# Performance work log

Hardware: AMD Instinct MI355X
Metric: run time of the kernel (lower is better)

The kernel has to match this reference:

```python
import jax, jax.numpy as jnp
import numpy as np

B, H, V, L, M, D, C = 64, 512, 50000, 400, 128, 64, 64
HC = 2 * D + M + 4  # controller LSTM hidden size (one head)
EPS = 1e-8


def _lstm_step(x, h, c, Wih, Whh, bih, bhh):
    g = x @ Wih.T + bih + h @ Whh.T + bhh
    i, f, gg, o = jnp.split(g, 4, axis=-1)
    c2 = jax.nn.sigmoid(f) * c + jax.nn.sigmoid(i) * jnp.tanh(gg)
    return jax.nn.sigmoid(o) * jnp.tanh(c2), c2


def _head_params(hc):
    # slices exactly as in LSTMMemoryController (k=0, single head)
    keys = hc[:, :M]                               # [B, M]
    kstr = jnp.exp(hc[:, D:D + 1])                 # [B, 1]
    gate = jax.nn.sigmoid(hc[:, D + 1:D + 2])      # [B, 1]
    erase = jax.nn.sigmoid(hc[:, D + 4:M + D + 4]) # [B, M]
    add = jax.nn.sigmoid(hc[:, 2 * D + 4:M + 2 * D + 4])  # [B, M]
    return keys, kstr, gate, erase, add


def _addressing(keys, kstr, gate, heads, memory):
    # torch cosine_similarity(keys.unsqueeze(2), memory, dim=2):
    # keys [B,M] broadcast along memory_dim D
    num = keys * memory.sum(-1)                                   # [B, M]
    nk = jnp.maximum(jnp.abs(keys) * jnp.sqrt(jnp.float32(D)), EPS)
    nm = jnp.maximum(jnp.linalg.norm(memory, axis=-1), EPS)
    cos = num / (nk * nm)
    content = jax.nn.softmax(kstr * cos, axis=1)                  # [B, M]
    # faithful to original: heads[k] indexes axis 0 (k=0) -> shape [1, M]
    gated = gate * content + (1.0 - gate) * heads[0]
    return gated[:, None, :]                                      # [B, 1, M]


def reference(input_ids, h0, c0, encoder_outputs, word_occurrence_indicator,
              coverage, memory, read_heads, write_heads,
              read_h, read_c, write_h, write_c,
              emb, attn_W, attn_b, cov_W, state_W, comb_W, comb_b,
              rpre_W, rpre_b, wpre_W, wpre_b,
              r_Wih, r_Whh, r_bih, r_bhh,
              w_Wih, w_Whh, w_bih, w_bhh,
              l_Wih, l_Whh, l_bih, l_bhh,
              out_W, out_b):
    embedded = emb[input_ids]                                     # [B, H]
    ia = jnp.concatenate([embedded, h0], 1) @ attn_W.T + attn_b  # [B, L]
    tc = (coverage + ia) @ cov_W.T
    ts = c0 @ state_W.T
    aw = jax.nn.softmax(tc + ia + ts, axis=1)                     # [B, L]
    attn_applied = jnp.einsum('bl,blh->bh', aw, encoder_outputs)  # [B, H]
    out0 = jnp.concatenate([embedded, attn_applied], 1) @ comb_W.T + comb_b  # [B, H]

    hm = jnp.concatenate([h0, memory.reshape(-1, M * D)], 1)
    rh, rc = _lstm_step(hm @ rpre_W.T + rpre_b, read_h, read_c, r_Wih, r_Whh, r_bih, r_bhh)
    wh, wc = _lstm_step(hm @ wpre_W.T + wpre_b, write_h, write_c, w_Wih, w_Whh, w_bih, w_bhh)
    rk, rks, rg, _, _ = _head_params(rh)
    wk, wks, wg, we, wa = _head_params(wh)
    rw = _addressing(rk, rks, rg, read_heads, memory)             # [B, 1, M]
    ww = _addressing(wk, wks, wg, write_heads, memory)            # [B, 1, M]

    read_in = jnp.einsum('bkm,bmd->bkd', rw, memory).reshape(-1, D)
    h1, c1 = _lstm_step(jnp.concatenate([out0, read_in], 1), h0, c0,
                        l_Wih, l_Whh, l_bih, l_bhh)
    # residual (h1 + out0) is computed in the original but unused by its output path

    w0 = ww[:, 0, :, None]                                        # [B, M, 1]
    new_memory = memory * (1.0 - w0 * we[:, :, None]) + w0 * wa[:, :, None]
    new_coverage = coverage + ia

    log_probs = jax.nn.log_softmax(c1[:, None, :] @ out_W.T + out_b, axis=-1)  # [B, 1, V]
    return log_probs, h1, c1, new_memory, new_coverage


def setup_inputs() -> dict:
    key = jax.random.key(0)
    ks = iter(jax.random.split(key, 48))

    def rn(shape, fan_in):
        return jax.random.normal(next(ks), shape, jnp.float32) / np.sqrt(fan_in)

    inp = {
        'input_ids': jax.random.randint(next(ks), (B,), 0, V),
        'h0': jax.random.normal(next(ks), (B, H), jnp.float32),
        'c0': jax.random.normal(next(ks), (B, H), jnp.float32),
        'encoder_outputs': jax.random.normal(next(ks), (B, L, H), jnp.float32),
        'word_occurrence_indicator': jnp.zeros((B, L), jnp.float32),
        'coverage': jnp.zeros((B, L), jnp.float32),
        'memory': jax.random.normal(next(ks), (B, M, D), jnp.float32),
        'read_heads': jnp.zeros((B, 1, M), jnp.float32),
        'write_heads': jnp.zeros((B, 1, M), jnp.float32),
        'read_h': jnp.zeros((B, HC), jnp.float32),
        'read_c': jnp.zeros((B, HC), jnp.float32),
        'write_h': jnp.zeros((B, HC), jnp.float32),
        'write_c': jnp.zeros((B, HC), jnp.float32),
        'emb': rn((V, H), H),
        'attn_W': rn((L, 2 * H), 2 * H), 'attn_b': jnp.zeros((L,), jnp.float32),
        'cov_W': rn((L, L), L),
        'state_W': rn((L, H), H),
        'comb_W': rn((H, 2 * H), 2 * H), 'comb_b': jnp.zeros((H,), jnp.float32),
        'rpre_W': rn((C, M * D + H), M * D + H), 'rpre_b': jnp.zeros((C,), jnp.float32),
        'wpre_W': rn((C, M * D + H), M * D + H), 'wpre_b': jnp.zeros((C,), jnp.float32),
        'r_Wih': rn((4 * HC, C), C), 'r_Whh': rn((4 * HC, HC), HC),
        'r_bih': jnp.zeros((4 * HC,), jnp.float32), 'r_bhh': jnp.zeros((4 * HC,), jnp.float32),
        'w_Wih': rn((4 * HC, C), C), 'w_Whh': rn((4 * HC, HC), HC),
        'w_bih': jnp.zeros((4 * HC,), jnp.float32), 'w_bhh': jnp.zeros((4 * HC,), jnp.float32),
        'l_Wih': rn((4 * H, H + D), H + D), 'l_Whh': rn((4 * H, H), H),
        'l_bih': jnp.zeros((4 * H,), jnp.float32), 'l_bhh': jnp.zeros((4 * H,), jnp.float32),
        'out_W': rn((V, H), H), 'out_b': jnp.zeros((V,), jnp.float32),
    }
    return inp
```

## Files before the change

kernel.cpp:

```cpp
#include <hip/hip_runtime.h>
#include <math.h>

#define BB 64
#define HH 512
#define VV 50000
#define LL 400
#define MM 128
#define DD 64
#define HC 260
#define EPSF 1e-8f

typedef __attribute__((ext_vector_type(8))) short bf16x8;
typedef __attribute__((ext_vector_type(4))) float f32x4;

__device__ __forceinline__ float sigmoidf(float x){ return 1.0f/(1.0f+expf(-x)); }
__device__ __forceinline__ unsigned short bf16_rne(float f){
  unsigned u = __float_as_uint(f);
  return (unsigned short)((u + 0x7fffu + ((u >> 16) & 1u)) >> 16);
}
__device__ __forceinline__ float wave_max(float v){
  #pragma unroll
  for(int o=32;o;o>>=1) v = fmaxf(v, __shfl_xor(v,o));
  return v;
}
__device__ __forceinline__ float wave_sum(float v){
  #pragma unroll
  for(int o=32;o;o>>=1) v += __shfl_xor(v,o);
  return v;
}

__global__ void k_embed(const int* __restrict__ ids, const float* __restrict__ emb,
                        const float* __restrict__ h0, float* __restrict__ xcat1,
                        float* __restrict__ xcat2){
  int idx = blockIdx.x*256 + threadIdx.x;
  if (idx >= BB*HH) return;
  int b = idx >> 9, h = idx & 511;
  float e = emb[(long)ids[b]*HH + h];
  xcat1[b*1024 + h] = e;
  xcat2[b*1024 + h] = e;
  xcat1[b*1024 + 512 + h] = h0[idx];
}

template<int NB, int FUSE>
__global__ __launch_bounds__(256) void k_gemv(const float* __restrict__ A,
                                              const float* __restrict__ A2,
                                              const float* __restrict__ W,
                                              const float* __restrict__ b1,
                                              float* __restrict__ C,
                                              int K, int N, int ldc){
  int b = blockIdx.y;
  int wid = threadIdx.x >> 6, lane = threadIdx.x & 63;
  int n = blockIdx.x*4 + wid;
  if (n >= N) return;
  const float4* A4  = (const float4*)(A + (long)b*K);
  const float4* A24 = (const float4*)(A2 + (long)b*K);
  const float4* W4  = (const float4*)(W + (long)n*K);
  int K4 = K >> 2;
  float acc = 0.f;
  for (int k = lane; k < K4; k += 64){
    float4 a = A4[k];
    if (FUSE){ float4 a2 = A24[k]; a.x+=a2.x; a.y+=a2.y; a.z+=a2.z; a.w+=a2.w; }
    float4 w = W4[k];
    acc += a.x*w.x + a.y*w.y + a.z*w.z + a.w*w.w;
  }
  acc = wave_sum(acc);
  if (lane == 0){
    if (NB) acc += b1[n];
    C[(long)b*ldc + n] = acc;
  }
}

__global__ void k_cov(const float* __restrict__ cov, const float* __restrict__ ia,
                      float* __restrict__ out){
  int idx = blockIdx.x*256 + threadIdx.x;
  if (idx >= BB*LL) return;
  out[idx] = cov[idx] + ia[idx];
}

__global__ __launch_bounds__(256) void k_softmax_aw(const float* __restrict__ ia,
                                                    const float* __restrict__ ts,
                                                    const float* __restrict__ tc,
                                                    float* __restrict__ aw){
  int b = blockIdx.x, t = threadIdx.x;
  int i0 = t, i1 = t + 256;
  float x0 = ia[b*LL+i0] + ts[b*LL+i0] + tc[b*LL+i0];
  float x1 = (i1 < LL) ? (ia[b*LL+i1] + ts[b*LL+i1] + tc[b*LL+i1]) : -INFINITY;
  __shared__ float sm[4], ss[4];
  float m = wave_max(fmaxf(x0, x1));
  if ((t & 63) == 0) sm[t>>6] = m;
  __syncthreads();
  m = fmaxf(fmaxf(sm[0], sm[1]), fmaxf(sm[2], sm[3]));
  float e0 = expf(x0 - m);
  float e1 = (i1 < LL) ? expf(x1 - m) : 0.0f;
  float s = wave_sum(e0 + e1);
  if ((t & 63) == 0) ss[t>>6] = s;
  __syncthreads();
  float tot = ss[0] + ss[1] + ss[2] + ss[3];
  float inv = 1.0f / tot;
  aw[b*LL + i0] = e0 * inv;
  if (i1 < LL) aw[b*LL + i1] = e1 * inv;
}

__global__ __launch_bounds__(256) void k_attn_part(const float* __restrict__ aw,
                                                   const float* __restrict__ enc,
                                                   float* __restrict__ part){
  int b = blockIdx.x, lc = blockIdx.y, t = threadIdx.x;
  const float* awb = aw + b*LL + lc*25;
  const float* eb  = enc + ((long)b*LL + lc*25)*HH;
  float a0 = 0.f, a1 = 0.f;
  for (int l = 0; l < 25; l++){
    float a = awb[l];
    a0 += a * eb[(long)l*HH + t];
    a1 += a * eb[(long)l*HH + t + 256];
  }
  part[((b*16 + lc) << 9) + t]       = a0;
  part[((b*16 + lc) << 9) + t + 256] = a1;
}

__global__ void k_attn_reduce(const float* __restrict__ part, float* __restrict__ xcat2){
  int idx = blockIdx.x*256 + threadIdx.x;
  if (idx >= BB*HH) return;
  int b = idx >> 9, h = idx & 511;
  float s = 0.f;
  #pragma unroll
  for (int lc = 0; lc < 16; lc++) s += part[((b*16 + lc) << 9) + h];
  xcat2[b*1024 + 512 + h] = s;
}

__global__ __launch_bounds__(256) void k_pre_gemv(const float* __restrict__ h0,
                                                  const float* __restrict__ mem,
                                                  const float* __restrict__ rW,
                                                  const float* __restrict__ wW,
                                                  float* __restrict__ part){
  int wid = threadIdx.x >> 6, lane = threadIdx.x & 63;
  int n = blockIdx.x*4 + wid;
  int b = blockIdx.y;
  int z = blockIdx.z;
  int which = z >> 3, chunk = z & 7;
  const float* W = which ? wW : rW;
  const float4* W4 = (const float4*)(W + (long)n*8704 + chunk*1088);
  const float4* H4 = (const float4*)(h0 + (long)b*HH);
  const float4* M4 = (const float4*)(mem + (long)b*8192 + (chunk*1088 - 512));
  float acc = 0.f;
  #pragma unroll
  for (int i = 0; i < 5; i++){
    int k4 = lane + i*64;
    if (k4 < 272){
      int kg4 = chunk*272 + k4;
      float4 a = (kg4 < 128) ? H4[kg4] : M4[k4];
      float4 w = W4[k4];
      acc += a.x*w.x + a.y*w.y + a.z*w.z + a.w*w.w;
    }
  }
  acc = wave_sum(acc);
  if (lane == 0) part[z*4096 + b*64 + n] = acc;
}

__global__ void k_pre_reduce(const float* __restrict__ part, const float* __restrict__ rb,
                             const float* __restrict__ wb, float* __restrict__ pre_r,
                             float* __restrict__ pre_w){
  int idx = blockIdx.x*256 + threadIdx.x;
  if (idx >= 8192) return;
  int which = idx >> 12;
  int r = idx & 4095;
  float s = 0.f;
  #pragma unroll
  for (int c = 0; c < 8; c++) s += part[((which<<3)+c)*4096 + r];
  int n = r & 63;
  s += which ? wb[n] : rb[n];
  (which ? pre_w : pre_r)[r] = s;
}

__global__ __launch_bounds__(256) void k_gates_rw(const float* __restrict__ pre_r,
    const float* __restrict__ pre_w, const float* __restrict__ read_h,
    const float* __restrict__ write_h,
    const float* __restrict__ rWih, const float* __restrict__ rWhh,
    const float* __restrict__ rbih, const float* __restrict__ rbhh,
    const float* __restrict__ wWih, const float* __restrict__ wWhh,
    const float* __restrict__ wbih, const float* __restrict__ wbhh,
    float* __restrict__ g_r, float* __restrict__ g_w){
  int which = blockIdx.z;
  int b = blockIdx.y;
  int wid = threadIdx.x >> 6, lane = threadIdx.x & 63;
  int n = blockIdx.x*4 + wid;
  const float* pre = which ? pre_w : pre_r;
  const float* hh  = which ? write_h : read_h;
  const float* Wih = which ? wWih : rWih;
  const float* Whh = which ? wWhh : rWhh;
  float acc = pre[b*64 + lane] * Wih[n*64 + lane];
  const float* hb = hh + b*HC;
  const float* wr = Whh + (long)n*HC;
  #pragma unroll
  for (int i = 0; i < 5; i++){
    int k = lane + i*64;
    if (k < HC) acc += hb[k]*wr[k];
  }
  acc = wave_sum(acc);
  if (lane == 0){
    acc += (which ? wbih : rbih)[n] + (which ? wbhh : rbhh)[n];
    (which ? g_w : g_r)[(long)b*4*HC + n] = acc;
  }
}

__global__ void k_lstm_rw(const float* __restrict__ g_r, const float* __restrict__ g_w,
                          const float* __restrict__ read_c, const float* __restrict__ write_c,
                          float* __restrict__ rh, float* __restrict__ wh){
  int idx = blockIdx.x*256 + threadIdx.x;
  if (idx >= 2*BB*HC) return;
  int which = idx >= BB*HC;
  int r = which ? idx - BB*HC : idx;
  int b = r / HC, j = r - b*HC;
  const float* g = (which ? g_w : g_r) + (long)b*4*HC;
  float c2 = sigmoidf(g[HC + j]) * (which ? write_c : read_c)[r]
           + sigmoidf(g[j]) * tanhf(g[2*HC + j]);
  (which ? wh : rh)[r] = sigmoidf(g[3*HC + j]) * tanhf(c2);
}

__global__ __launch_bounds__(128) void k_address(const float* __restrict__ rh,
                                                 const float* __restrict__ whv,
                                                 const float* __restrict__ rheads,
                                                 const float* __restrict__ wheads,
                                                 const float* __restrict__ mem,
                                                 float* __restrict__ rwout,
                                                 float* __restrict__ wwout){
  int which = blockIdx.y;
  int b = blockIdx.x, m = threadIdx.x;
  const float* hc = which ? whv : rh;
  const float* heads0 = which ? wheads : rheads;
  float* wout = which ? wwout : rwout;
  const float* mr = mem + ((long)b*MM + m)*DD;
  float s = 0.f, q = 0.f;
  #pragma unroll 8
  for (int d = 0; d < DD; d++){ float v = mr[d]; s += v; q += v*v; }
  float key  = hc[b*HC + m];
  float kstr = expf(hc[b*HC + 64]);
  float gate = sigmoidf(hc[b*HC + 65]);
  float nk = fmaxf(fabsf(key)*8.0f, EPSF);
  float nm = fmaxf(sqrtf(q), EPSF);
  float z  = kstr * (key*s) / (nk*nm);
  __shared__ float sm[2], ss[2];
  float mx = wave_max(z);
  if ((m & 63) == 0) sm[m>>6] = mx;
  __syncthreads();
  mx = fmaxf(sm[0], sm[1]);
  float e = expf(z - mx);
  float w = wave_sum(e);
  if ((m & 63) == 0) ss[m>>6] = w;
  __syncthreads();
  float content = e / (ss[0] + ss[1]);
  wout[b*MM + m] = gate*content + (1.0f - gate)*heads0[m];
}

__global__ void k_readin(const float* __restrict__ rw, const float* __restrict__ mem,
                         float* __restrict__ xcat3){
  int b = blockIdx.x, d = threadIdx.x;
  float s = 0.f;
  for (int m = 0; m < MM; m++) s += rw[b*MM + m] * mem[((long)b*MM + m)*DD + d];
  xcat3[b*576 + 512 + d] = s;
}

__global__ void k_newmem(const float* __restrict__ mem, const float* __restrict__ ww,
                         const float* __restrict__ wh, float* __restrict__ out){
  int idx = blockIdx.x*256 + threadIdx.x;
  if (idx >= BB*MM*DD) return;
  int b = idx >> 13;
  int m = (idx & 8191) >> 6;
  float w0 = ww[b*MM + m];
  float we = sigmoidf(wh[b*HC + 68 + m]);
  float wa = sigmoidf(wh[b*HC + 132 + m]);
  out[idx] = mem[idx]*(1.0f - w0*we) + w0*wa;
}

__global__ __launch_bounds__(256) void k_lstm_main(const float* __restrict__ xcat3,
                                                   const float* __restrict__ h0,
                                                   const float* __restrict__ lWih,
                                                   const float* __restrict__ lWhh,
                                                   const float* __restrict__ bih,
                                                   const float* __restrict__ bhh,
                                                   const float* __restrict__ c0,
                                                   float* __restrict__ h1,
                                                   float* __restrict__ c1,
                                                   unsigned short* __restrict__ c1b){
  int wid = threadIdx.x >> 6, lane = threadIdx.x & 63;
  int j = blockIdx.x*4 + wid;
  int b = blockIdx.y;
  const float4* A1 = (const float4*)(xcat3 + (long)b*576);
  const float4* A2 = (const float4*)(h0 + (long)b*HH);
  float gv[4];
  #pragma unroll
  for (int g = 0; g < 4; g++){
    int n = g*HH + j;
    const float4* W1 = (const float4*)(lWih + (long)n*576);
    const float4* W2 = (const float4*)(lWhh + (long)n*HH);
    float s = 0.f;
    #pragma unroll
    for (int i = 0; i < 3; i++){
      int k = lane + i*64;
      if (k < 144){ float4 a = A1[k], w = W1[k]; s += a.x*w.x + a.y*w.y + a.z*w.z + a.w*w.w; }
    }
    #pragma unroll
    for (int i = 0; i < 2; i++){
      int k = lane + i*64;
      float4 a = A2[k], w = W2[k]; s += a.x*w.x + a.y*w.y + a.z*w.z + a.w*w.w;
    }
    gv[g] = wave_sum(s);
  }
  if (lane == 0){
    #pragma unroll
    for (int g = 0; g < 4; g++){ int n = g*HH + j; gv[g] += bih[n] + bhh[n]; }
    float c2 = sigmoidf(gv[1])*c0[b*HH + j] + sigmoidf(gv[0])*tanhf(gv[2]);
    h1[b*HH + j] = sigmoidf(gv[3])*tanhf(c2);
    c1[b*HH + j] = c2;
    c1b[b*HH + j] = bf16_rne(c2);
  }
}

__global__ __launch_bounds__(256) void k_logits_mfma(const unsigned short* __restrict__ Ab,
                                                     const float* __restrict__ W,
                                                     const float* __restrict__ bias,
                                                     float* __restrict__ C){
  int wid = threadIdx.x >> 6, lane = threadIdx.x & 63;
  int strip = blockIdx.x*4 + wid;
  if (strip >= 3125) return;
  int nl = lane & 15;
  int q  = lane >> 4;
  int n  = strip*16 + nl;
  const float* wrow = W + (long)n*HH + q*8;
  const unsigned short* a0p = Ab + (0*16 + nl)*HH + q*8;
  const unsigned short* a1p = Ab + (1*16 + nl)*HH + q*8;
  const unsigned short* a2p = Ab + (2*16 + nl)*HH + q*8;
  const unsigned short* a3p = Ab + (3*16 + nl)*HH + q*8;
  f32x4 acc0 = {0.f,0.f,0.f,0.f}, acc1 = acc0, acc2 = acc0, acc3 = acc0;
  #pragma unroll 4
  for (int ks = 0; ks < 16; ks++){
    const float4* wp = (const float4*)(wrow + ks*32);
    float4 w0 = wp[0];
    float4 w1 = wp[1];
    bf16x8 bf;
    bf[0] = (short)bf16_rne(w0.x); bf[1] = (short)bf16_rne(w0.y);
    bf[2] = (short)bf16_rne(w0.z); bf[3] = (short)bf16_rne(w0.w);
    bf[4] = (short)bf16_rne(w1.x); bf[5] = (short)bf16_rne(w1.y);
    bf[6] = (short)bf16_rne(w1.z); bf[7] = (short)bf16_rne(w1.w);
    bf16x8 a0 = *(const bf16x8*)(a0p + ks*32);
    bf16x8 a1 = *(const bf16x8*)(a1p + ks*32);
    bf16x8 a2 = *(const bf16x8*)(a2p + ks*32);
    bf16x8 a3 = *(const bf16x8*)(a3p + ks*32);
    acc0 = __builtin_amdgcn_mfma_f32_16x16x32_bf16(a0, bf, acc0, 0, 0, 0);
    acc1 = __builtin_amdgcn_mfma_f32_16x16x32_bf16(a1, bf, acc1, 0, 0, 0);
    acc2 = __builtin_amdgcn_mfma_f32_16x16x32_bf16(a2, bf, acc2, 0, 0, 0);
    acc3 = __builtin_amdgcn_mfma_f32_16x16x32_bf16(a3, bf, acc3, 0, 0, 0);
  }
  float bv = bias[n];
  #pragma unroll
  for (int r = 0; r < 4; r++){
    int m = q*4 + r;
    C[(long)(m     )*VV + n] = acc0[r] + bv;
    C[(long)(m + 16)*VV + n] = acc1[r] + bv;
    C[(long)(m + 32)*VV + n] = acc2[r] + bv;
    C[(long)(m + 48)*VV + n] = acc3[r] + bv;
  }
}

__global__ __launch_bounds__(256) void k_ls1(const float* __restrict__ lp,
                                             float* __restrict__ pm, float* __restrict__ ps){
  int b = blockIdx.y, c = blockIdx.x, t = threadIdx.x;
  const float* row = lp + (long)b*VV + c*2000;
  float mx = -INFINITY;
  for (int i = t; i < 2000; i += 256) mx = fmaxf(mx, row[i]);
  __shared__ float sm[4], ss[4];
  mx = wave_max(mx);
  if ((t & 63) == 0) sm[t>>6] = mx;
  __syncthreads();
  mx = fmaxf(fmaxf(sm[0], sm[1]), fmaxf(sm[2], sm[3]));
  float s = 0.f;
  for (int i = t; i < 2000; i += 256) s += expf(row[i] - mx);
  s = wave_sum(s);
  if ((t & 63) == 0) ss[t>>6] = s;
  __syncthreads();
  if (t == 0){ pm[b*25 + c] = mx; ps[b*25 + c] = ss[0]+ss[1]+ss[2]+ss[3]; }
}

__global__ void k_ls2(const float* __restrict__ pm, const float* __restrict__ ps,
                      float* __restrict__ lse){
  int b = threadIdx.x;
  float m = -INFINITY;
  for (int c = 0; c < 25; c++) m = fmaxf(m, pm[b*25 + c]);
  float s = 0.f;
  for (int c = 0; c < 25; c++) s += ps[b*25 + c]*expf(pm[b*25 + c] - m);
  lse[b] = m + logf(s);
}

__global__ void k_ls3(float* __restrict__ lp, const float* __restrict__ lse){
  int idx = blockIdx.x*256 + threadIdx.x;
  if (idx >= BB*VV) return;
  int b = idx / VV;
  lp[idx] -= lse[b];
}

extern "C" void kernel_launch(void* const* d_in, const int* in_sizes, int n_in,
                              void* d_out, int out_size, void* d_ws, size_t ws_size,
                              hipStream_t stream) {
  const int*   ids     = (const int*)  d_in[0];
  const float* h0      = (const float*)d_in[1];
  const float* c0      = (const float*)d_in[2];
  const float* enc     = (const float*)d_in[3];
  const float* cov     = (const float*)d_in[5];
  const float* mem     = (const float*)d_in[6];
  const float* rheads  = (const float*)d_in[7];
  const float* wheads  = (const float*)d_in[8];
  const float* read_h  = (const float*)d_in[9];
  const float* read_c  = (const float*)d_in[10];
  const float* write_h = (const float*)d_in[11];
  const float* write_c = (const float*)d_in[12];
  const float* emb     = (const float*)d_in[13];
  const float* attn_W  = (const float*)d_in[14];
  const float* attn_b  = (const float*)d_in[15];
  const float* cov_W   = (const float*)d_in[16];
  const float* state_W = (const float*)d_in[17];
  const float* comb_W  = (const float*)d_in[18];
  const float* comb_b  = (const float*)d_in[19];
  const float* rpre_W  = (const float*)d_in[20];
  const float* rpre_b  = (const float*)d_in[21];
  const float* wpre_W  = (const float*)d_in[22];
  const float* wpre_b  = (const float*)d_in[23];
  const float* r_Wih   = (const float*)d_in[24];
  const float* r_Whh   = (const float*)d_in[25];
  const float* r_bih   = (const float*)d_in[26];
  const float* r_bhh   = (const float*)d_in[27];
  const float* w_Wih   = (const float*)d_in[28];
  const float* w_Whh   = (const float*)d_in[29];
  const float* w_bih   = (const float*)d_in[30];
  const float* w_bhh   = (const float*)d_in[31];
  const float* l_Wih   = (const float*)d_in[32];
  const float* l_Whh   = (const float*)d_in[33];
  const float* l_bih   = (const float*)d_in[34];
  const float* l_bhh   = (const float*)d_in[35];
  const float* out_W   = (const float*)d_in[36];
  const float* out_b   = (const float*)d_in[37];

  float* out  = (float*)d_out;
  float* lp   = out;
  float* h1   = out + 3200000;
  float* c1   = h1 + 32768;
  float* nmem = c1 + 32768;
  float* ncov = nmem + 524288;

  float* w = (float*)d_ws;
  float* xcat1 = w;
  float* xcat2 = xcat1 + 65536;
  float* xcat3 = xcat2 + 65536;
  float* ia    = xcat3 + 36864;
  float* ts    = ia + 25600;
  float* tc    = ts + 25600;
  float* aw    = tc + 25600;
  float* U     = aw + 25600;
  float* pre_r = U + 557056;
  float* pre_w = pre_r + 4096;
  float* g_r   = pre_w + 4096;
  float* g_w   = g_r + 66560;
  float* rh    = g_w + 66560;
  float* wh    = rh + 16640;
  float* rw    = wh + 16640;
  float* wwgt  = rw + 8192;
  float* pm    = wwgt + 8192;
  float* ps    = pm + 1600;
  float* lse   = ps + 1600;
  unsigned short* c1b = (unsigned short*)(lse + 64);

  k_embed<<<128, 256, 0, stream>>>(ids, emb, h0, xcat1, xcat2);
  k_gemv<1,0><<<dim3(100,64), 256, 0, stream>>>(xcat1, xcat1, attn_W, attn_b, ia, 1024, LL, LL);
  k_gemv<0,0><<<dim3(100,64), 256, 0, stream>>>(c0, c0, state_W, nullptr, ts, HH, LL, LL);
  k_cov<<<100, 256, 0, stream>>>(cov, ia, ncov);
  k_gemv<0,1><<<dim3(100,64), 256, 0, stream>>>(cov, ia, cov_W, nullptr, tc, LL, LL, LL);
  k_softmax_aw<<<64, 256, 0, stream>>>(ia, ts, tc, aw);
  k_attn_part<<<dim3(64,16), 256, 0, stream>>>(aw, enc, U);
  k_attn_reduce<<<128, 256, 0, stream>>>(U, xcat2);
  k_gemv<1,0><<<dim3(128,64), 256, 0, stream>>>(xcat2, xcat2, comb_W, comb_b, xcat3, 1024, HH, 576);

  k_pre_gemv<<<dim3(16,64,16), 256, 0, stream>>>(h0, mem, rpre_W, wpre_W, U);
  k_pre_reduce<<<32, 256, 0, stream>>>(U, rpre_b, wpre_b, pre_r, pre_w);

  k_gates_rw<<<dim3(260,64,2), 256, 0, stream>>>(pre_r, pre_w, read_h, write_h,
      r_Wih, r_Whh, r_bih, r_bhh, w_Wih, w_Whh, w_bih, w_bhh, g_r, g_w);
  k_lstm_rw<<<130, 256, 0, stream>>>(g_r, g_w, read_c, write_c, rh, wh);

  k_address<<<dim3(64,2), 128, 0, stream>>>(rh, wh, rheads, wheads, mem, rw, wwgt);
  k_readin<<<64, 64, 0, stream>>>(rw, mem, xcat3);
  k_newmem<<<2048, 256, 0, stream>>>(mem, wwgt, wh, nmem);

  k_lstm_main<<<dim3(128,64), 256, 0, stream>>>(xcat3, h0, l_Wih, l_Whh, l_bih, l_bhh,
                                                c0, h1, c1, c1b);

  k_logits_mfma<<<782, 256, 0, stream>>>(c1b, out_W, out_b, lp);
  k_ls1<<<dim3(25,64), 256, 0, stream>>>(lp, pm, ps);
  k_ls2<<<1, 64, 0, stream>>>(pm, ps, lse);
  k_ls3<<<12500, 256, 0, stream>>>(lp, lse);
}
```

Before: 503.7 us.

## Fuse small kernels, batch gate GEMV, and software-pipeline logits MFMA loads

Folds the coverage update into the attention softmax, merges addressing with the read-in and memory-update kernels, and merges the two-stage log-sum-exp finish into the final subtract kernel, which cuts four launches. The gate GEMV now reuses register-held weights across 8 batch rows per block. The logits MFMA loop prefetches weights and activations two steps ahead with a 3-slot register ring. The trade-offs are more register pressure in the logits kernel and the read-in and memory-update work running on only 128 blocks.

```diff
diff --git a/kernel.cpp b/kernel.cpp
--- a/kernel.cpp
+++ b/kernel.cpp
@@ -70,21 +70,20 @@
   }
 }
 
-__global__ void k_cov(const float* __restrict__ cov, const float* __restrict__ ia,
-                      float* __restrict__ out){
-  int idx = blockIdx.x*256 + threadIdx.x;
-  if (idx >= BB*LL) return;
-  out[idx] = cov[idx] + ia[idx];
-}
-
 __global__ __launch_bounds__(256) void k_softmax_aw(const float* __restrict__ ia,
                                                     const float* __restrict__ ts,
                                                     const float* __restrict__ tc,
-                                                    float* __restrict__ aw){
+                                                    const float* __restrict__ cov,
+                                                    float* __restrict__ aw,
+                                                    float* __restrict__ ncov){
   int b = blockIdx.x, t = threadIdx.x;
   int i0 = t, i1 = t + 256;
-  float x0 = ia[b*LL+i0] + ts[b*LL+i0] + tc[b*LL+i0];
-  float x1 = (i1 < LL) ? (ia[b*LL+i1] + ts[b*LL+i1] + tc[b*LL+i1]) : -INFINITY;
+  float ia0 = ia[b*LL+i0];
+  float x0 = ia0 + ts[b*LL+i0] + tc[b*LL+i0];
+  float ia1 = (i1 < LL) ? ia[b*LL+i1] : 0.f;
+  float x1 = (i1 < LL) ? (ia1 + ts[b*LL+i1] + tc[b*LL+i1]) : -INFINITY;
+  ncov[b*LL + i0] = cov[b*LL + i0] + ia0;
+  if (i1 < LL) ncov[b*LL + i1] = cov[b*LL + i1] + ia1;
   __shared__ float sm[4], ss[4];
   float m = wave_max(fmaxf(x0, x1));
   if ((t & 63) == 0) sm[t>>6] = m;
@@ -180,25 +179,35 @@
     const float* __restrict__ wbih, const float* __restrict__ wbhh,
     float* __restrict__ g_r, float* __restrict__ g_w){
   int which = blockIdx.z;
-  int b = blockIdx.y;
+  int bo = blockIdx.y;
   int wid = threadIdx.x >> 6, lane = threadIdx.x & 63;
   int n = blockIdx.x*4 + wid;
   const float* pre = which ? pre_w : pre_r;
   const float* hh  = which ? write_h : read_h;
   const float* Wih = which ? wWih : rWih;
   const float* Whh = which ? wWhh : rWhh;
-  float acc = pre[b*64 + lane] * Wih[n*64 + lane];
-  const float* hb = hh + b*HC;
+  float* gout = which ? g_w : g_r;
+  float wih_l = Wih[(long)n*64 + lane];
   const float* wr = Whh + (long)n*HC;
+  float whh_l[5];
   #pragma unroll
   for (int i = 0; i < 5; i++){
     int k = lane + i*64;
-    if (k < HC) acc += hb[k]*wr[k];
-  }
-  acc = wave_sum(acc);
-  if (lane == 0){
-    acc += (which ? wbih : rbih)[n] + (which ? wbhh : rbhh)[n];
-    (which ? g_w : g_r)[(long)b*4*HC + n] = acc;
+    whh_l[i] = (k < HC) ? wr[k] : 0.f;
+  }
+  float bsum = (which ? wbih : rbih)[n] + (which ? wbhh : rbhh)[n];
+  #pragma unroll
+  for (int i = 0; i < 8; i++){
+    int b = bo*8 + i;
+    float acc = pre[b*64 + lane] * wih_l;
+    const float* hb = hh + (long)b*HC;
+    #pragma unroll
+    for (int j = 0; j < 5; j++){
+      int k = lane + j*64;
+      if (k < HC) acc += whh_l[j]*hb[k];
+    }
+    acc = wave_sum(acc);
+    if (lane == 0) gout[(long)b*4*HC + n] = acc + bsum;
   }
 }
 
@@ -221,13 +230,12 @@
                                                  const float* __restrict__ rheads,
                                                  const float* __restrict__ wheads,
                                                  const float* __restrict__ mem,
-                                                 float* __restrict__ rwout,
-                                                 float* __restrict__ wwout){
+                                                 float* __restrict__ xcat3,
+                                                 float* __restrict__ nmem){
   int which = blockIdx.y;
   int b = blockIdx.x, m = threadIdx.x;
   const float* hc = which ? whv : rh;
   const float* heads0 = which ? wheads : rheads;
-  float* wout = which ? wwout : rwout;
   const float* mr = mem + ((long)b*MM + m)*DD;
   float s = 0.f, q = 0.f;
   #pragma unroll 8
@@ -239,36 +247,42 @@
   float nm = fmaxf(sqrtf(q), EPSF);
   float z  = kstr * (key*s) / (nk*nm);
   __shared__ float sm[2], ss[2];
+  __shared__ float sw[128];
   float mx = wave_max(z);
   if ((m & 63) == 0) sm[m>>6] = mx;
   __syncthreads();
   mx = fmaxf(sm[0], sm[1]);
   float e = expf(z - mx);
-  float w = wave_sum(e);
-  if ((m & 63) == 0) ss[m>>6] = w;
+  float wsum = wave_sum(e);
+  if ((m & 63) == 0) ss[m>>6] = wsum;
   __syncthreads();
   float content = e / (ss[0] + ss[1]);
-  wout[b*MM + m] = gate*content + (1.0f - gate)*heads0[m];
-}
-
-__global__ void k_readin(const float* __restrict__ rw, const float* __restrict__ mem,
-                         float* __restrict__ xcat3){
-  int b = blockIdx.x, d = threadIdx.x;
-  float s = 0.f;
-  for (int m = 0; m < MM; m++) s += rw[b*MM + m] * mem[((long)b*MM + m)*DD + d];
-  xcat3[b*576 + 512 + d] = s;
-}
-
-__global__ void k_newmem(const float* __restrict__ mem, const float* __restrict__ ww,
-                         const float* __restrict__ wh, float* __restrict__ out){
-  int idx = blockIdx.x*256 + threadIdx.x;
-  if (idx >= BB*MM*DD) return;
-  int b = idx >> 13;
-  int m = (idx & 8191) >> 6;
-  float w0 = ww[b*MM + m];
-  float we = sigmoidf(wh[b*HC + 68 + m]);
-  float wa = sigmoidf(wh[b*HC + 132 + m]);
-  out[idx] = mem[idx]*(1.0f - w0*we) + w0*wa;
+  float w = gate*content + (1.0f - gate)*heads0[m];
+  if (which == 0){
+    sw[m] = w;
+    __syncthreads();
+    if (m < 64){
+      float acc = 0.f;
+      const float* mb = mem + (long)b*MM*DD + m;
+      #pragma unroll 8
+      for (int mm = 0; mm < MM; mm++) acc += sw[mm]*mb[(long)mm*DD];
+      xcat3[b*576 + 512 + m] = acc;
+    }
+  } else {
+    float we = sigmoidf(hc[b*HC + 68 + m]);
+    float wa = sigmoidf(hc[b*HC + 132 + m]);
+    float scale = 1.0f - w*we;
+    float addv  = w*wa;
+    const float4* mr4 = (const float4*)mr;
+    float4* out4 = (float4*)(nmem + ((long)b*MM + m)*DD);
+    #pragma unroll
+    for (int d4 = 0; d4 < 16; d4++){
+      float4 v = mr4[d4];
+      v.x = v.x*scale + addv; v.y = v.y*scale + addv;
+      v.z = v.z*scale + addv; v.w = v.w*scale + addv;
+      out4[d4] = v;
+    }
+  }
 }
 
 __global__ __launch_bounds__(256) void k_lstm_main(const float* __restrict__ xcat3,
@@ -325,30 +339,38 @@
   int nl = lane & 15;
   int q  = lane >> 4;
   int n  = strip*16 + nl;
-  const float* wrow = W + (long)n*HH + q*8;
-  const unsigned short* a0p = Ab + (0*16 + nl)*HH + q*8;
-  const unsigned short* a1p = Ab + (1*16 + nl)*HH + q*8;
-  const unsigned short* a2p = Ab + (2*16 + nl)*HH + q*8;
-  const unsigned short* a3p = Ab + (3*16 + nl)*HH + q*8;
+  const float4* wp  = (const float4*)(W + (long)n*HH + q*8);
+  const bf16x8* a0p = (const bf16x8*)(Ab + (long)nl*HH + q*8);
+  const bf16x8* a1p = (const bf16x8*)(Ab + (long)(16+nl)*HH + q*8);
+  const bf16x8* a2p = (const bf16x8*)(Ab + (long)(32+nl)*HH + q*8);
+  const bf16x8* a3p = (const bf16x8*)(Ab + (long)(48+nl)*HH + q*8);
   f32x4 acc0 = {0.f,0.f,0.f,0.f}, acc1 = acc0, acc2 = acc0, acc3 = acc0;
-  #pragma unroll 4
+  float4 wA[3], wB[3];
+  bf16x8 fa0[3], fa1[3], fa2[3], fa3[3];
+  #pragma unroll
+  for (int p = 0; p < 2; p++){
+    wA[p] = wp[p*8]; wB[p] = wp[p*8 + 1];
+    fa0[p] = a0p[p*4]; fa1[p] = a1p[p*4];
+    fa2[p] = a2p[p*4]; fa3[p] = a3p[p*4];
+  }
+  #pragma unroll
   for (int ks = 0; ks < 16; ks++){
-    const float4* wp = (const float4*)(wrow + ks*32);
-    float4 w0 = wp[0];
-    float4 w1 = wp[1];
+    int cur = ks % 3;
+    if (ks < 14){
+      int nx = (ks + 2) % 3;
+      wA[nx] = wp[(ks+2)*8]; wB[nx] = wp[(ks+2)*8 + 1];
+      fa0[nx] = a0p[(ks+2)*4]; fa1[nx] = a1p[(ks+2)*4];
+      fa2[nx] = a2p[(ks+2)*4]; fa3[nx] = a3p[(ks+2)*4];
+    }
     bf16x8 bf;
-    bf[0] = (short)bf16_rne(w0.x); bf[1] = (short)bf16_rne(w0.y);
-    bf[2] = (short)bf16_rne(w0.z); bf[3] = (short)bf16_rne(w0.w);
-    bf[4] = (short)bf16_rne(w1.x); bf[5] = (short)bf16_rne(w1.y);
-    bf[6] = (short)bf16_rne(w1.z); bf[7] = (short)bf16_rne(w1.w);
-    bf16x8 a0 = *(const bf16x8*)(a0p + ks*32);
-    bf16x8 a1 = *(const bf16x8*)(a1p + ks*32);
-    bf16x8 a2 = *(const bf16x8*)(a2p + ks*32);
-    bf16x8 a3 = *(const bf16x8*)(a3p + ks*32);
-    acc0 = __builtin_amdgcn_mfma_f32_16x16x32_bf16(a0, bf, acc0, 0, 0, 0);
-    acc1 = __builtin_amdgcn_mfma_f32_16x16x32_bf16(a1, bf, acc1, 0, 0, 0);
-    acc2 = __builtin_amdgcn_mfma_f32_16x16x32_bf16(a2, bf, acc2, 0, 0, 0);
-    acc3 = __builtin_amdgcn_mfma_f32_16x16x32_bf16(a3, bf, acc3, 0, 0, 0);
+    bf[0] = (short)bf16_rne(wA[cur].x); bf[1] = (short)bf16_rne(wA[cur].y);
+    bf[2] = (short)bf16_rne(wA[cur].z); bf[3] = (short)bf16_rne(wA[cur].w);
+    bf[4] = (short)bf16_rne(wB[cur].x); bf[5] = (short)bf16_rne(wB[cur].y);
+    bf[6] = (short)bf16_rne(wB[cur].z); bf[7] = (short)bf16_rne(wB[cur].w);
+    acc0 = __builtin_amdgcn_mfma_f32_16x16x32_bf16(fa0[cur], bf, acc0, 0, 0, 0);
+    acc1 = __builtin_amdgcn_mfma_f32_16x16x32_bf16(fa1[cur], bf, acc1, 0, 0, 0);
+    acc2 = __builtin_amdgcn_mfma_f32_16x16x32_bf16(fa2[cur], bf, acc2, 0, 0, 0);
+    acc3 = __builtin_amdgcn_mfma_f32_16x16x32_bf16(fa3[cur], bf, acc3, 0, 0, 0);
   }
   float bv = bias[n];
   #pragma unroll
@@ -380,21 +402,19 @@
   if (t == 0){ pm[b*25 + c] = mx; ps[b*25 + c] = ss[0]+ss[1]+ss[2]+ss[3]; }
 }
 
-__global__ void k_ls2(const float* __restrict__ pm, const float* __restrict__ ps,
-                      float* __restrict__ lse){
-  int b = threadIdx.x;
+__global__ __launch_bounds__(256) void k_ls3(float* __restrict__ lp,
+                                             const float* __restrict__ pm,
+                                             const float* __restrict__ ps){
+  int b = blockIdx.y, c = blockIdx.x, t = threadIdx.x;
   float m = -INFINITY;
-  for (int c = 0; c < 25; c++) m = fmaxf(m, pm[b*25 + c]);
+  #pragma unroll
+  for (int k = 0; k < 25; k++) m = fmaxf(m, pm[b*25 + k]);
   float s = 0.f;
-  for (int c = 0; c < 25; c++) s += ps[b*25 + c]*expf(pm[b*25 + c] - m);
-  lse[b] = m + logf(s);
-}
-
-__global__ void k_ls3(float* __restrict__ lp, const float* __restrict__ lse){
-  int idx = blockIdx.x*256 + threadIdx.x;
-  if (idx >= BB*VV) return;
-  int b = idx / VV;
-  lp[idx] -= lse[b];
+  #pragma unroll
+  for (int k = 0; k < 25; k++) s += ps[b*25 + k]*expf(pm[b*25 + k] - m);
+  float lse = m + logf(s);
+  int i = c*256 + t;
+  if (i < VV) lp[(long)b*VV + i] -= lse;
 }
 
 extern "C" void kernel_launch(void* const* d_in, const int* in_sizes, int n_in,
@@ -460,19 +480,15 @@
   float* g_w   = g_r + 66560;
   float* rh    = g_w + 66560;
   float* wh    = rh + 16640;
-  float* rw    = wh + 16640;
-  float* wwgt  = rw + 8192;
-  float* pm    = wwgt + 8192;
+  float* pm    = wh + 16640;
   float* ps    = pm + 1600;
-  float* lse   = ps + 1600;
-  unsigned short* c1b = (unsigned short*)(lse + 64);
+  unsigned short* c1b = (unsigned short*)(ps + 1600);
 
   k_embed<<<128, 256, 0, stream>>>(ids, emb, h0, xcat1, xcat2);
   k_gemv<1,0><<<dim3(100,64), 256, 0, stream>>>(xcat1, xcat1, attn_W, attn_b, ia, 1024, LL, LL);
   k_gemv<0,0><<<dim3(100,64), 256, 0, stream>>>(c0, c0, state_W, nullptr, ts, HH, LL, LL);
-  k_cov<<<100, 256, 0, stream>>>(cov, ia, ncov);
   k_gemv<0,1><<<dim3(100,64), 256, 0, stream>>>(cov, ia, cov_W, nullptr, tc, LL, LL, LL);
-  k_softmax_aw<<<64, 256, 0, stream>>>(ia, ts, tc, aw);
+  k_softmax_aw<<<64, 256, 0, stream>>>(ia, ts, tc, cov, aw, ncov);
   k_attn_part<<<dim3(64,16), 256, 0, stream>>>(aw, enc, U);
   k_attn_reduce<<<128, 256, 0, stream>>>(U, xcat2);
   k_gemv<1,0><<<dim3(128,64), 256, 0, stream>>>(xcat2, xcat2, comb_W, comb_b, xcat3, 1024, HH, 576);
@@ -480,19 +496,16 @@
   k_pre_gemv<<<dim3(16,64,16), 256, 0, stream>>>(h0, mem, rpre_W, wpre_W, U);
   k_pre_reduce<<<32, 256, 0, stream>>>(U, rpre_b, wpre_b, pre_r, pre_w);
 
-  k_gates_rw<<<dim3(260,64,2), 256, 0, stream>>>(pre_r, pre_w, read_h, write_h,
+  k_gates_rw<<<dim3(260,8,2), 256, 0, stream>>>(pre_r, pre_w, read_h, write_h,
       r_Wih, r_Whh, r_bih, r_bhh, w_Wih, w_Whh, w_bih, w_bhh, g_r, g_w);
   k_lstm_rw<<<130, 256, 0, stream>>>(g_r, g_w, read_c, write_c, rh, wh);
 
-  k_address<<<dim3(64,2), 128, 0, stream>>>(rh, wh, rheads, wheads, mem, rw, wwgt);
-  k_readin<<<64, 64, 0, stream>>>(rw, mem, xcat3);
-  k_newmem<<<2048, 256, 0, stream>>>(mem, wwgt, wh, nmem);
+  k_address<<<dim3(64,2), 128, 0, stream>>>(rh, wh, rheads, wheads, mem, xcat3, nmem);
 
   k_lstm_main<<<dim3(128,64), 256, 0, stream>>>(xcat3, h0, l_Wih, l_Whh, l_bih, l_bhh,
                                                 c0, h1, c1, c1b);
 
   k_logits_mfma<<<782, 256, 0, stream>>>(c1b, out_W, out_b, lp);
   k_ls1<<<dim3(25,64), 256, 0, stream>>>(lp, pm, ps);
-  k_ls2<<<1, 64, 0, stream>>>(pm, ps, lse);
-  k_ls3<<<12500, 256, 0, stream>>>(lp, lse);
-}
+  k_ls3<<<dim3(196,64), 256, 0, stream>>>(lp, pm, ps);
+}
```

Result: no change. 510.7 us (+1.4%).
